# Performance work log

Measured on AMD Instinct MI355X. Metric: run time of the kernel, lower is better.

## Reference

```python
import jax, jax.numpy as jnp
import numpy as np

B, C, H, W = 8, 64, 64, 64


def setup_inputs() -> dict:
    key = jax.random.key(0)
    ks = jax.random.split(key, 8)
    s = 1.0 / np.sqrt(C)  # keep logits in a reasonable range
    return {
        "x": jax.random.normal(ks[0], (B, C, H, W), dtype=jnp.float32),
        "Wf": jax.random.normal(ks[1], (C, C), dtype=jnp.float32) * s,
        "bf": jax.random.normal(ks[2], (C,), dtype=jnp.float32) * s,
        "Wg": jax.random.normal(ks[3], (C, C), dtype=jnp.float32) * s,
        "bg": jax.random.normal(ks[4], (C,), dtype=jnp.float32) * s,
        "Wh": jax.random.normal(ks[5], (C, C), dtype=jnp.float32) * s,
        "bh": jax.random.normal(ks[6], (C,), dtype=jnp.float32) * s,
        "gamma": jax.random.normal(ks[7], (1,), dtype=jnp.float32),
    }


def reference(x, Wf, bf, Wg, bg, Wh, bh, gamma):
    b, c, h, w = x.shape
    n = h * w
    xf = x.reshape(b, c, n)  # [B, C, N]
    # 1x1 convs == per-pixel channel GEMMs
    f = jnp.einsum("oc,bcn->bon", Wf, xf) + bf[None, :, None]  # [B, C, N]
    g = jnp.einsum("oc,bcn->bon", Wg, xf) + bg[None, :, None]
    hh = jnp.einsum("oc,bcn->bon", Wh, xf) + bh[None, :, None]
    # att_in[b, i, j] = f[b, :, i] . g[b, :, j]  (f_x permuted then bmm with g_x)
    att = jax.nn.softmax(jnp.einsum("bci,bcj->bij", f, g), axis=-1)  # [B, N, N]
    # torch.bmm(h_x, attention): out[b, c, j] = sum_i h[b, c, i] * att[b, i, j]
    out = jnp.einsum("bci,bij->bcj", hh, att).reshape(b, c, h, w)
    return gamma[0] * out + x
```

## Files before the change

kernel.cpp:

```cpp
#include <hip/hip_runtime.h>

#define BB 8
#define CC 64
#define NN 4096
#define NIC 4
#define JCH 8
#define LOG2E 1.4426950408889634f

typedef float f32x4  __attribute__((ext_vector_type(4)));
typedef float f32x16 __attribute__((ext_vector_type(16)));
typedef _Float16 half8_t __attribute__((ext_vector_type(8)));
typedef int int4v __attribute__((ext_vector_type(4)));


__global__ __launch_bounds__(64) void qkv_kernel(
    const float* __restrict__ x,
    const float* __restrict__ Wf, const float* __restrict__ bf,
    const float* __restrict__ Wg, const float* __restrict__ bg,
    const float* __restrict__ Wh, const float* __restrict__ bh,
    _Float16* __restrict__ fT, _Float16* __restrict__ gT,
    _Float16* __restrict__ hT)
{
    const int split = blockIdx.x;
    const int z     = split >> 2;
    const int o0    = (split & 3) * 16;
    const int n     = blockIdx.y * 64 + threadIdx.x;
    const int b     = blockIdx.z;
    const float* W    = (z == 0) ? Wf : ((z == 1) ? Wg : Wh);
    const float* bias = (z == 0) ? bf : ((z == 1) ? bg : bh);

    float xv[CC];
    const float* xp = x + (size_t)b * CC * NN + n;
#pragma unroll
    for (int c = 0; c < CC; ++c) xv[c] = xp[(size_t)c * NN];

    if (z < 2) {
        _Float16* dst = ((z == 0) ? fT : gT) + (size_t)(b * NN + n) * CC + o0;
        const float scale = (z == 0) ? LOG2E : 1.0f;
#pragma unroll
        for (int o8 = 0; o8 < 2; ++o8) {
            half8_t v;
#pragma unroll
            for (int oo = 0; oo < 8; ++oo) {
                const int o = o0 + o8 * 8 + oo;
                float acc = bias[o];
#pragma unroll
                for (int c = 0; c < CC; ++c) acc += W[o * CC + c] * xv[c];
                v[oo] = (_Float16)(acc * scale);
            }
            *(half8_t*)(dst + o8 * 8) = v;
        }
    } else {
        _Float16* hdst = hT + ((size_t)(b * (NN / 32) + (n >> 5)) * CC) * 32 + (n & 31);
#pragma unroll
        for (int o = o0; o < o0 + 16; ++o) {
            float acc = bias[o];
#pragma unroll
            for (int c = 0; c < CC; ++c) acc += W[o * CC + c] * xv[c];
            hdst[o * 32] = (_Float16)acc;
        }
    }
}

__global__ __launch_bounds__(256, 4) void stats_kernel(
    const _Float16* __restrict__ fT, const _Float16* __restrict__ gT,
    float* __restrict__ lpart)
{
    __shared__ _Float16 gbuf[2][64][72];

    const int lane = threadIdx.x & 63;
    const int wv   = threadIdx.x >> 6;
    const int b    = blockIdx.y;
    const int jc   = blockIdx.z;
    const int i0   = blockIdx.x * 128 + wv * 32;
    const int l31  = lane & 31;
    const int q5   = lane >> 5;

    half8_t a[4];
    const _Float16* fa = fT + (size_t)(b * NN + i0 + l31) * CC + q5 * 8;
#pragma unroll
    for (int kc = 0; kc < 4; ++kc) a[kc] = *(const half8_t*)(fa + kc * 16);

    const _Float16* gchunk = gT + (size_t)(b * NN + jc * (NN / JCH)) * CC;
    const int T = NN / JCH / 64;

    const int srow = wv * 16 + (lane >> 3);
    const int scol = (lane & 7) * 8;

    {
        const half8_t v0 = *(const half8_t*)(gchunk + (size_t)srow * CC + scol);
        const half8_t v1 = *(const half8_t*)(gchunk + (size_t)(srow + 8) * CC + scol);
        *(half8_t*)&gbuf[0][srow][scol] = v0;
        *(half8_t*)&gbuf[0][srow + 8][scol] = v1;
    }
    __syncthreads();

    float l16[16];
#pragma unroll
    for (int r = 0; r < 16; ++r) l16[r] = 0.f;

    for (int t = 0; t < T; ++t) {
        const int buf = t & 1;
        const bool pf = (t + 1 < T);
        half8_t p0, p1;
        if (pf) {
            const _Float16* src = gchunk + (size_t)((t + 1) * 64 + srow) * CC + scol;
            p0 = *(const half8_t*)(src);
            p1 = *(const half8_t*)(src + 8 * CC);
        }
#pragma unroll
        for (int js = 0; js < 2; ++js) {
            const _Float16* grow = &gbuf[buf][js * 32 + l31][0] + q5 * 8;
            f32x16 s = {};
#pragma unroll
            for (int kc = 0; kc < 4; ++kc) {
                const half8_t bfr = *(const half8_t*)(grow + kc * 16);
                s = __builtin_amdgcn_mfma_f32_32x32x16_f16(a[kc], bfr, s, 0, 0, 0);
            }
#pragma unroll
            for (int r = 0; r < 16; ++r) l16[r] += __builtin_exp2f(s[r]);
        }
        if (pf) {
            *(half8_t*)&gbuf[buf ^ 1][srow][scol] = p0;
            *(half8_t*)&gbuf[buf ^ 1][srow + 8][scol] = p1;
        }
        __syncthreads();
    }

#pragma unroll
    for (int r = 0; r < 16; ++r) {
#pragma unroll
        for (int off = 1; off < 32; off <<= 1)
            l16[r] += __shfl_xor(l16[r], off);
    }

    if (l31 == 0) {
        float* lp = lpart + (size_t)jc * BB * NN + b * NN + i0;
#pragma unroll
        for (int rb = 0; rb < 4; ++rb) {
            f32x4 v;
#pragma unroll
            for (int k = 0; k < 4; ++k) v[k] = l16[rb * 4 + k];
            *(f32x4*)(lp + rb * 8 + q5 * 4) = v;
        }
    }
}

__global__ __launch_bounds__(256) void rmerge_kernel(
    const float* __restrict__ lpart, float* __restrict__ nbias)
{
    const int idx = blockIdx.x * 256 + threadIdx.x;
    float s = 0.f;
#pragma unroll
    for (int jc = 0; jc < JCH; ++jc) s += lpart[(size_t)jc * BB * NN + idx];
    nbias[idx] = -__builtin_log2f(s);
}

__global__ __launch_bounds__(256, 4) void attn_kernel(
    const _Float16* __restrict__ fT, const _Float16* __restrict__ gT,
    const _Float16* __restrict__ hT, const float* __restrict__ nbias,
    _Float16* __restrict__ pout)
{
    __shared__ _Float16 fbuf[2][64][72];
    __shared__ _Float16 hbuf[2][64][72];

    const int lane = threadIdx.x & 63;
    const int wv   = threadIdx.x >> 6;
    const int b    = blockIdx.y;
    const int ic   = blockIdx.z;
    const int l31  = lane & 31;
    const int q5   = lane >> 5;
    const int j    = blockIdx.x * 128 + wv * 32 + l31;

    half8_t bg[4];
    const _Float16* grow = gT + (size_t)(b * NN + j) * CC + q5 * 8;
#pragma unroll
    for (int kc = 0; kc < 4; ++kc) bg[kc] = *(const half8_t*)(grow + kc * 16);

    f32x16 acc[2] = {};

    const int ichunk = NN / NIC;
    const int ibase  = ic * ichunk;
    const _Float16* fchunk = fT + ((size_t)b * NN + ibase) * CC;
    const _Float16* hchunk = hT + ((size_t)(b * (NN / 32) + ibase / 32) * CC) * 32;
    const float*    nb     = nbias + b * NN + ibase;
    const int T = ichunk / 64;

    const int tid    = threadIdx.x;
    const int frow_s = tid >> 2;
    const int fcol_s = (tid & 3) * 16;
    const int hrow_s = tid >> 2;
    const int hcol_s = (tid & 3) * 8;

    {
        const half8_t f0 = *(const half8_t*)(fchunk + (size_t)frow_s * CC + fcol_s);
        const half8_t f1 = *(const half8_t*)(fchunk + (size_t)frow_s * CC + fcol_s + 8);
        const half8_t h0 = *(const half8_t*)(hchunk + tid * 8);
        const half8_t h1 = *(const half8_t*)(hchunk + 2048 + tid * 8);
        *(half8_t*)&fbuf[0][frow_s][fcol_s]     = f0;
        *(half8_t*)&fbuf[0][frow_s][fcol_s + 8] = f1;
        *(half8_t*)&hbuf[0][hrow_s][hcol_s]      = h0;
        *(half8_t*)&hbuf[0][hrow_s][32 + hcol_s] = h1;
    }
    __syncthreads();

    for (int t = 0; t < T; ++t) {
        const int buf = t & 1;
        const bool pf = (t + 1 < T);
        half8_t pf0, pf1, ph0, ph1;
        if (pf) {
            const _Float16* fsrc = fchunk + (size_t)((t + 1) * 64 + frow_s) * CC + fcol_s;
            const _Float16* hsrc = hchunk + (size_t)(t + 1) * 4096 + tid * 8;
            pf0 = *(const half8_t*)(fsrc);
            pf1 = *(const half8_t*)(fsrc + 8);
            ph0 = *(const half8_t*)(hsrc);
            ph1 = *(const half8_t*)(hsrc + 2048);
        }

#pragma unroll
        for (int ih = 0; ih < 2; ++ih) {
            f32x16 s;
#pragma unroll
            for (int rb = 0; rb < 4; ++rb) {
                const f32x4 n4 = *(const f32x4*)(nb + t * 64 + ih * 32 + rb * 8 + q5 * 4);
#pragma unroll
                for (int k = 0; k < 4; ++k) s[rb * 4 + k] = n4[k];
            }
            const _Float16* frow = &fbuf[buf][ih * 32 + l31][0] + q5 * 8;
#pragma unroll
            for (int kc = 0; kc < 4; ++kc) {
                const half8_t af = *(const half8_t*)(frow + kc * 16);
                s = __builtin_amdgcn_mfma_f32_32x32x16_f16(af, bg[kc], s, 0, 0, 0);
            }

            int e[8];
#pragma unroll
            for (int r8 = 0; r8 < 8; ++r8) {
                e[r8] = __builtin_bit_cast(int, __builtin_amdgcn_cvt_pkrtz(
                    __builtin_exp2f(s[r8 * 2]), __builtin_exp2f(s[r8 * 2 + 1])));
            }

            const int sA = q5 ? e[0] : e[2];
            const int sB = q5 ? e[1] : e[3];
            const int sC = q5 ? e[4] : e[6];
            const int sD = q5 ? e[5] : e[7];
            const int rA = __shfl_xor(sA, 32, 64);
            const int rB = __shfl_xor(sB, 32, 64);
            const int rC = __shfl_xor(sC, 32, 64);
            const int rD = __shfl_xor(sD, 32, 64);
            int4v b0, b1;
            b0[0] = q5 ? rA   : e[0];
            b0[1] = q5 ? rB   : e[1];
            b0[2] = q5 ? e[2] : rA;
            b0[3] = q5 ? e[3] : rB;
            b1[0] = q5 ? rC   : e[4];
            b1[1] = q5 ? rD   : e[5];
            b1[2] = q5 ? e[6] : rC;
            b1[3] = q5 ? e[7] : rD;
            const half8_t B0 = __builtin_bit_cast(half8_t, b0);
            const half8_t B1 = __builtin_bit_cast(half8_t, b1);

#pragma unroll
            for (int ct = 0; ct < 2; ++ct) {
                const half8_t ah0 = *(const half8_t*)(&hbuf[buf][ct * 32 + l31][0] + ih * 32 + q5 * 8);
                acc[ct] = __builtin_amdgcn_mfma_f32_32x32x16_f16(ah0, B0, acc[ct], 0, 0, 0);
            }
#pragma unroll
            for (int ct = 0; ct < 2; ++ct) {
                const half8_t ah1 = *(const half8_t*)(&hbuf[buf][ct * 32 + l31][0] + ih * 32 + 16 + q5 * 8);
                acc[ct] = __builtin_amdgcn_mfma_f32_32x32x16_f16(ah1, B1, acc[ct], 0, 0, 0);
            }
        }

        if (pf) {
            *(half8_t*)&fbuf[buf ^ 1][frow_s][fcol_s]     = pf0;
            *(half8_t*)&fbuf[buf ^ 1][frow_s][fcol_s + 8] = pf1;
            *(half8_t*)&hbuf[buf ^ 1][hrow_s][hcol_s]      = ph0;
            *(half8_t*)&hbuf[buf ^ 1][hrow_s][32 + hcol_s] = ph1;
        }
        __syncthreads();
    }

    _Float16* pb_out = pout + (((size_t)ic * BB + b) * CC) * NN;
#pragma unroll
    for (int ct = 0; ct < 2; ++ct) {
#pragma unroll
        for (int r = 0; r < 16; ++r) {
            const int c = ct * 32 + (r & 3) + 8 * (r >> 2) + 4 * q5;
            pb_out[(size_t)c * NN + j] = (_Float16)acc[ct][r];
        }
    }
}

__global__ __launch_bounds__(256) void combine_kernel(
    const float* __restrict__ x, const float* __restrict__ gammap,
    const _Float16* __restrict__ pout, float* __restrict__ out)
{
    const float gam = gammap[0];
    const size_t i8 = ((size_t)blockIdx.x * 256 + threadIdx.x) * 8;
    const size_t TOT = (size_t)BB * CC * NN;

    float s[8] = {0.f, 0.f, 0.f, 0.f, 0.f, 0.f, 0.f, 0.f};
#pragma unroll
    for (int ic = 0; ic < NIC; ++ic) {
        const half8_t p = *(const half8_t*)(pout + ic * TOT + i8);
#pragma unroll
        for (int k = 0; k < 8; ++k) s[k] += (float)p[k];
    }
    const f32x4 x0 = *(const f32x4*)(x + i8);
    const f32x4 x1 = *(const f32x4*)(x + i8 + 4);
    f32x4 o0, o1;
#pragma unroll
    for (int k = 0; k < 4; ++k) { o0[k] = gam * s[k] + x0[k]; o1[k] = gam * s[k + 4] + x1[k]; }
    *(f32x4*)(out + i8) = o0;
    *(f32x4*)(out + i8 + 4) = o1;
}

extern "C" void kernel_launch(void* const* d_in, const int* in_sizes, int n_in,
                              void* d_out, int out_size, void* d_ws, size_t ws_size,
                              hipStream_t stream) {
    const float* x     = (const float*)d_in[0];
    const float* Wf    = (const float*)d_in[1];
    const float* bf    = (const float*)d_in[2];
    const float* Wg    = (const float*)d_in[3];
    const float* bg    = (const float*)d_in[4];
    const float* Wh    = (const float*)d_in[5];
    const float* bh    = (const float*)d_in[6];
    const float* gamma = (const float*)d_in[7];
    float* out = (float*)d_out;

    const size_t TOT = (size_t)BB * CC * NN;
    _Float16* fT   = (_Float16*)d_ws;
    _Float16* gT   = fT + TOT;
    _Float16* hT   = gT + TOT;
    _Float16* pout = hT + TOT;
    float* lpart   = (float*)(pout + (size_t)NIC * TOT);
    float* nbias   = lpart + (size_t)JCH * BB * NN;

    qkv_kernel<<<dim3(12, NN / 64, BB), 64, 0, stream>>>(
        x, Wf, bf, Wg, bg, Wh, bh, fT, gT, hT);
    stats_kernel<<<dim3(NN / 128, BB, JCH), 256, 0, stream>>>(fT, gT, lpart);
    rmerge_kernel<<<dim3(BB * NN / 256), 256, 0, stream>>>(lpart, nbias);
    attn_kernel<<<dim3(NN / 128, BB, NIC), 256, 0, stream>>>(fT, gT, hT, nbias, pout);
    combine_kernel<<<dim3(TOT / (256 * 8)), 256, 0, stream>>>(x, gamma, pout, out);
}
```

Measured before the change: 200.0 us.

## Compute QKV projections with fp16 MFMA using LDS-staged input tiles

Rewrites the 1x1-conv projection kernel to stage a 64x128 input tile in shared memory and compute the channel GEMM with 32x32x16 fp16 MFMA instructions instead of scalar FMA loops over per-thread register arrays. The launch grid changes to 128-pixel blocks of 256 threads, with one block per projection. The goal is to cut the scalar-ALU cost and the redundant x reloads of the QKV stage. In exchange, x and the weights are rounded to fp16 before the multiply, which lowers projection precision, and the fT/gT outputs are now written as scattered 2-byte stores.

```diff
diff --git a/kernel.cpp b/kernel.cpp
--- a/kernel.cpp
+++ b/kernel.cpp
@@ -13,7 +13,7 @@
 typedef int int4v __attribute__((ext_vector_type(4)));
 
 
-__global__ __launch_bounds__(64) void qkv_kernel(
+__global__ __launch_bounds__(256, 4) void qkv_kernel(
     const float* __restrict__ x,
     const float* __restrict__ Wf, const float* __restrict__ bf,
     const float* __restrict__ Wg, const float* __restrict__ bg,
@@ -21,43 +21,96 @@
     _Float16* __restrict__ fT, _Float16* __restrict__ gT,
     _Float16* __restrict__ hT)
 {
-    const int split = blockIdx.x;
-    const int z     = split >> 2;
-    const int o0    = (split & 3) * 16;
-    const int n     = blockIdx.y * 64 + threadIdx.x;
-    const int b     = blockIdx.z;
+    __shared__ float xbuf[64][136];
+
+    const int tid  = threadIdx.x;
+    const int lane = tid & 63;
+    const int wv   = tid >> 6;
+    const int l31  = lane & 31;
+    const int q5   = lane >> 5;
+    const int n0   = blockIdx.x * 128;
+    const int b    = blockIdx.y;
+    const int z    = blockIdx.z;
     const float* W    = (z == 0) ? Wf : ((z == 1) ? Wg : Wh);
     const float* bias = (z == 0) ? bf : ((z == 1) ? bg : bh);
 
-    float xv[CC];
-    const float* xp = x + (size_t)b * CC * NN + n;
-#pragma unroll
-    for (int c = 0; c < CC; ++c) xv[c] = xp[(size_t)c * NN];
+    {
+        const int row = tid >> 2;
+        const float* src = x + (size_t)(b * CC + row) * NN + n0 + (tid & 3) * 4;
+#pragma unroll
+        for (int k = 0; k < 8; ++k) {
+            const f32x4 v = *(const f32x4*)(src + k * 16);
+            *(f32x4*)&xbuf[row][(tid & 3) * 4 + k * 16] = v;
+        }
+    }
+    __syncthreads();
+
+    const int px = wv * 32 + l31;
+    half8_t xf[4];
+#pragma unroll
+    for (int kc = 0; kc < 4; ++kc) {
+        const int kb = kc * 16 + q5 * 8;
+        int4v p;
+#pragma unroll
+        for (int h2 = 0; h2 < 4; ++h2) {
+            p[h2] = __builtin_bit_cast(int, __builtin_amdgcn_cvt_pkrtz(
+                xbuf[kb + h2 * 2][px], xbuf[kb + h2 * 2 + 1][px]));
+        }
+        xf[kc] = __builtin_bit_cast(half8_t, p);
+    }
+
+    half8_t wf[2][4];
+#pragma unroll
+    for (int ot = 0; ot < 2; ++ot) {
+        const float* wrow = W + (size_t)(ot * 32 + l31) * CC;
+#pragma unroll
+        for (int kc = 0; kc < 4; ++kc) {
+            const f32x4 w0 = *(const f32x4*)(wrow + kc * 16 + q5 * 8);
+            const f32x4 w1 = *(const f32x4*)(wrow + kc * 16 + q5 * 8 + 4);
+            int4v p;
+            p[0] = __builtin_bit_cast(int, __builtin_amdgcn_cvt_pkrtz(w0[0], w0[1]));
+            p[1] = __builtin_bit_cast(int, __builtin_amdgcn_cvt_pkrtz(w0[2], w0[3]));
+            p[2] = __builtin_bit_cast(int, __builtin_amdgcn_cvt_pkrtz(w1[0], w1[1]));
+            p[3] = __builtin_bit_cast(int, __builtin_amdgcn_cvt_pkrtz(w1[2], w1[3]));
+            wf[ot][kc] = __builtin_bit_cast(half8_t, p);
+        }
+    }
 
     if (z < 2) {
-        _Float16* dst = ((z == 0) ? fT : gT) + (size_t)(b * NN + n) * CC + o0;
         const float scale = (z == 0) ? LOG2E : 1.0f;
-#pragma unroll
-        for (int o8 = 0; o8 < 2; ++o8) {
-            half8_t v;
-#pragma unroll
-            for (int oo = 0; oo < 8; ++oo) {
-                const int o = o0 + o8 * 8 + oo;
-                float acc = bias[o];
-#pragma unroll
-                for (int c = 0; c < CC; ++c) acc += W[o * CC + c] * xv[c];
-                v[oo] = (_Float16)(acc * scale);
-            }
-            *(half8_t*)(dst + o8 * 8) = v;
+        _Float16* dstT = (z == 0) ? fT : gT;
+#pragma unroll
+        for (int ot = 0; ot < 2; ++ot) {
+            f32x16 acc = {};
+#pragma unroll
+            for (int kc = 0; kc < 4; ++kc)
+                acc = __builtin_amdgcn_mfma_f32_32x32x16_f16(xf[kc], wf[ot][kc], acc, 0, 0, 0);
+            const float bv = bias[ot * 32 + l31];
+#pragma unroll
+            for (int r = 0; r < 16; ++r) {
+                const int prow = (r & 3) + 8 * (r >> 2) + 4 * q5;
+                const int n = n0 + wv * 32 + prow;
+                dstT[(size_t)(b * NN + n) * CC + ot * 32 + l31] =
+                    (_Float16)((acc[r] + bv) * scale);
+            }
         }
     } else {
-        _Float16* hdst = hT + ((size_t)(b * (NN / 32) + (n >> 5)) * CC) * 32 + (n & 31);
-#pragma unroll
-        for (int o = o0; o < o0 + 16; ++o) {
-            float acc = bias[o];
-#pragma unroll
-            for (int c = 0; c < CC; ++c) acc += W[o * CC + c] * xv[c];
-            hdst[o * 32] = (_Float16)acc;
+        _Float16* hbase = hT + ((size_t)(b * (NN / 32) + (n0 + wv * 32) / 32) * CC) * 32;
+#pragma unroll
+        for (int ot = 0; ot < 2; ++ot) {
+            f32x16 acc = {};
+#pragma unroll
+            for (int kc = 0; kc < 4; ++kc)
+                acc = __builtin_amdgcn_mfma_f32_32x32x16_f16(wf[ot][kc], xf[kc], acc, 0, 0, 0);
+#pragma unroll
+            for (int rb = 0; rb < 4; ++rb) {
+                const f32x4 b4 = *(const f32x4*)(bias + ot * 32 + rb * 8 + q5 * 4);
+#pragma unroll
+                for (int k = 0; k < 4; ++k) {
+                    const int c = ot * 32 + rb * 8 + q5 * 4 + k;
+                    hbase[(size_t)c * 32 + l31] = (_Float16)(acc[rb * 4 + k] + b4[k]);
+                }
+            }
         }
     }
 }
@@ -337,7 +390,7 @@
     float* lpart   = (float*)(pout + (size_t)NIC * TOT);
     float* nbias   = lpart + (size_t)JCH * BB * NN;
 
-    qkv_kernel<<<dim3(12, NN / 64, BB), 64, 0, stream>>>(
+    qkv_kernel<<<dim3(NN / 128, BB, 3), 256, 0, stream>>>(
         x, Wf, bf, Wg, bg, Wh, bh, fT, gT, hT);
     stats_kernel<<<dim3(NN / 128, BB, JCH), 256, 0, stream>>>(fT, gT, lpart);
     rmerge_kernel<<<dim3(BB * NN / 256), 256, 0, stream>>>(lpart, nbias);
```

New measurement: 177.2 us. -11.4%, faster.
